# Optimization experiments

Measured on AMD Instinct MI355X. Metric: run time of the kernel, lower is better.

## Reference

```python
import jax, jax.numpy as jnp
import numpy as np

B, N, D = 32, 181, 512          # batch, num_projs (seq len), embed_dim
H, HD = 8, 64                   # heads, head_dim
DEPTH, FFN = 6, 2048            # layers, mlp_ratio*embed_dim
MAXLEN = 181                    # RPE max_len (EncoderLayer default)
LN_EPS = 1e-5


def setup_inputs() -> dict:
    key = jax.random.key(0)
    ks = jax.random.split(key, 16)
    rn = lambda k, s, sc=0.02: (jax.random.normal(k, s, jnp.float32) * sc)
    return {
        "x_0": jax.random.normal(ks[0], (B, N, D), jnp.float32),
        "max_shift": 50,
        "pos_embed": rn(ks[1], (1, N, D)),
        "qkv_w": rn(ks[2], (DEPTH, D, 3 * D)), "qkv_b": jnp.zeros((DEPTH, 3 * D), jnp.float32),
        "out_w": rn(ks[3], (DEPTH, D, D)), "out_b": jnp.zeros((DEPTH, D), jnp.float32),
        "rel_pos": jax.random.normal(ks[4], (DEPTH, 2 * MAXLEN - 1, HD), jnp.float32),
        "rpe_w": rn(ks[5], (DEPTH, HD, 1)),
        "ln1_g": jnp.ones((DEPTH, D), jnp.float32), "ln1_b": jnp.zeros((DEPTH, D), jnp.float32),
        "ffn_w1": rn(ks[6], (DEPTH, D, FFN)), "ffn_b1": jnp.zeros((DEPTH, FFN), jnp.float32),
        "ffn_w2": rn(ks[7], (DEPTH, FFN, D)), "ffn_b2": jnp.zeros((DEPTH, D), jnp.float32),
        "ln2_g": jnp.ones((DEPTH, D), jnp.float32), "ln2_b": jnp.zeros((DEPTH, D), jnp.float32),
        "mlp_w1": rn(ks[8], (D, 64)), "mlp_b1": jnp.zeros((64,), jnp.float32),
        "mlp_w2": rn(ks[9], (64, 1)), "mlp_b2": jnp.zeros((1,), jnp.float32),
    }


def _layer_norm(x, g, b):
    m = jnp.mean(x, -1, keepdims=True)
    v = jnp.mean((x - m) ** 2, -1, keepdims=True)
    return (x - m) * jax.lax.rsqrt(v + LN_EPS) * g + b


def reference(x_0, max_shift, pos_embed, qkv_w, qkv_b, out_w, out_b, rel_pos, rpe_w,
              ln1_g, ln1_b, ffn_w1, ffn_b1, ffn_w2, ffn_b2, ln2_g, ln2_b,
              mlp_w1, mlp_b1, mlp_w2, mlp_b2):
    Bb, T, L = x_0.shape
    n_head = H
    hd = L // n_head
    scale = hd ** -0.5
    max_len = (rel_pos.shape[1] + 1) // 2
    # relative position index table [T, T]
    idx = jnp.arange(T)[None, :] - jnp.arange(T)[:, None] + (max_len - 1)

    x = x_0 + pos_embed
    depth = qkv_w.shape[0]
    for i in range(depth):
        # --- MHA with relative position bias ---
        qkv = (x @ qkv_w[i] + qkv_b[i]).reshape(Bb, T, 3, n_head, hd)
        q, k, v = qkv[:, :, 0], qkv[:, :, 1], qkv[:, :, 2]   # [B,T,H,hd]
        scores = jnp.einsum('bqhd,bkhd->bhqk', q, k) * scale
        bias = (rel_pos[i][idx] @ rpe_w[i])[..., 0]          # [T,T]
        scores = scores + bias[None, None]
        w = jax.nn.softmax(scores, axis=-1)
        attn = jnp.einsum('bhqk,bkhd->bqhd', w, v).reshape(Bb, T, L)
        attn = attn @ out_w[i] + out_b[i]
        x = _layer_norm(x + attn, ln1_g[i], ln1_b[i])
        # --- FFN ---
        h = jax.nn.gelu(x @ ffn_w1[i] + ffn_b1[i], approximate=False)
        h = h @ ffn_w2[i] + ffn_b2[i]
        x = _layer_norm(x + h, ln2_g[i], ln2_b[i])

    # per-projection shift head
    shift = jax.nn.relu(x @ mlp_w1 + mlp_b1) @ mlp_w2 + mlp_b2   # [B,T,1]

    # --- SpatialTransformer: bilinear warp along L only (flow[:,0] == 0) ---
    grid_y = 2.0 * (jnp.arange(T, dtype=jnp.float32) / (T - 1) - 0.5)   # [T]
    grid_x = 2.0 * (jnp.arange(L, dtype=jnp.float32) / (L - 1) - 0.5)   # [L]
    flow_x = shift * max_shift / (L // 2)                               # [B,T,1]
    gx = grid_x[None, None, :] + flow_x                                 # [B,T,L]
    # unnormalize (align_corners=False), border padding -> clamp coords
    ix = jnp.clip(((gx + 1.0) * L - 1.0) / 2.0, 0.0, L - 1.0)
    iy = jnp.clip(((grid_y + 1.0) * T - 1.0) / 2.0, 0.0, T - 1.0)       # [T]
    ix0f = jnp.floor(ix); wx = ix - ix0f
    iy0f = jnp.floor(iy); wy = iy - iy0f
    ix0 = jnp.clip(ix0f.astype(jnp.int32), 0, L - 1)
    ix1 = jnp.clip(ix0 + 1, 0, L - 1)
    iy0 = jnp.clip(iy0f.astype(jnp.int32), 0, T - 1)
    iy1 = jnp.clip(iy0 + 1, 0, T - 1)
    bidx = jnp.arange(Bb)[:, None, None]
    iy0b, iy1b = iy0[None, :, None], iy1[None, :, None]
    v00 = x_0[bidx, iy0b, ix0]; v01 = x_0[bidx, iy0b, ix1]
    v10 = x_0[bidx, iy1b, ix0]; v11 = x_0[bidx, iy1b, ix1]
    wyb = wy[None, :, None]
    warped = (1 - wyb) * ((1 - wx) * v00 + wx * v01) + wyb * ((1 - wx) * v10 + wx * v11)
    return shift, warped
```

## Files before the change

kernel.cpp:

```cpp
#include <hip/hip_runtime.h>
#include <hip/hip_bf16.h>
#include <math.h>

#define M_ROWS 5792
#define NTOK 181
#define NLAYER 6

typedef __attribute__((ext_vector_type(8))) _Float16 f16x8;
typedef __attribute__((ext_vector_type(4))) float f32x4;
typedef __attribute__((ext_vector_type(16))) float f32x16;

__device__ __forceinline__ ushort f2h(float f) {
    union { _Float16 h; ushort u; } v;
    v.h = (_Float16)f;
    return v.u;
}
__device__ __forceinline__ float h2f(ushort u) {
    union { ushort u; _Float16 h; } v; v.u = u;
    return (float)v.h;
}
__device__ __forceinline__ float gelu_f(float v) {
    return 0.5f * v * (1.0f + erff(v * 0.70710678118654752f));
}
__device__ __forceinline__ void async16(const void* g, void* l) {
    __builtin_amdgcn_global_load_lds((const __attribute__((address_space(1))) void*)g,
                                     (__attribute__((address_space(3))) void*)l, 16, 0, 0);
}

__global__ __launch_bounds__(256) void wt_kernel(const float* __restrict__ W,
                                                 ushort* __restrict__ Wt, int K, int N) {
    __shared__ float t[64][65];
    const size_t ls = (size_t)blockIdx.z * K * N;
    const float* Wl = W + ls;
    ushort* Wtl = Wt + ls;
    const int k0 = blockIdx.x * 64, n0 = blockIdx.y * 64;
    const int tr = threadIdx.x >> 6, tc = threadIdx.x & 63;
    #pragma unroll
    for (int i = 0; i < 16; ++i) {
        const int r = i * 4 + tr;
        t[r][tc] = Wl[(size_t)(k0 + r) * N + n0 + tc];
    }
    __syncthreads();
    #pragma unroll
    for (int i = 0; i < 16; ++i) {
        const int r = i * 4 + tr;
        Wtl[(size_t)(n0 + r) * K + k0 + tc] = f2h(t[tc][r]);
    }
}

__global__ void add_pos_kernel(const float* __restrict__ x0, const float* __restrict__ pos,
                               float* __restrict__ x, ushort* __restrict__ xb) {
    int idx = blockIdx.x * 256 + threadIdx.x;
    const int total = M_ROWS * 128;
    if (idx >= total) return;
    int col = idx & 127;
    int m   = idx >> 7;
    int t   = m % NTOK;
    float4 a = ((const float4*)x0)[idx];
    float4 p = ((const float4*)pos)[t * 128 + col];
    a.x += p.x; a.y += p.y; a.z += p.z; a.w += p.w;
    ((float4*)x)[idx] = a;
    ((ushort4*)xb)[idx] = make_ushort4(f2h(a.x), f2h(a.y), f2h(a.z), f2h(a.w));
}

template<int BM, int EPI, int SK>
__global__ __launch_bounds__(256) void mfma_gemm(const ushort* __restrict__ A,
                                                 const ushort* __restrict__ Bt,
                                                 const float* __restrict__ bias,
                                                 void* __restrict__ Cv,
                                                 int M, int K, int N) {
    constexpr int MREP = BM / 32;
    __shared__ __align__(16) ushort sA[2][BM * 32];
    __shared__ __align__(16) ushort sB[2][128 * 32];

    const int NC  = N >> 7;
    const int NR  = (M + BM - 1) / BM;
    const int NRP = (NR + 7) & ~7;
    const int PSB = NRP * NC;
    const int gid = blockIdx.x;
    const int sk  = (SK > 1) ? gid / PSB : 0;
    const int j   = (SK > 1) ? gid % PSB : gid;
    const int r   = (j / (8 * NC)) * 8 + (j & 7);
    const int c   = (j % (8 * NC)) >> 3;
    if (r >= NR) return;

    const int tid = threadIdx.x;
    const int lane = tid & 63;
    const int w = tid >> 6;
    const int wr = w >> 1, wc = w & 1;
    const int row0 = r * BM, col0 = c * 128;
    const int wbase = tid & ~63;

    f32x4 acc[MREP][4];
    const f32x4 zero = {0.f, 0.f, 0.f, 0.f};
    #pragma unroll
    for (int m = 0; m < MREP; ++m)
        #pragma unroll
        for (int n = 0; n < 4; ++n) acc[m][n] = zero;

    auto stage = [&](int buf, int kt) {
        const int k0 = kt << 5;
        #pragma unroll
        for (int i = 0; i < BM / 64; ++i) {
            const int s = i * 256 + tid;
            const int row = s >> 2;
            const int kbl = (s & 3) ^ ((row >> 1) & 3);
            int gr = row0 + row; if (gr > M - 1) gr = M - 1;
            async16(A + (size_t)gr * K + k0 + (kbl << 3),
                    &sA[buf][(i * 256 + wbase) * 8]);
        }
        #pragma unroll
        for (int i = 0; i < 2; ++i) {
            const int s = i * 256 + tid;
            const int nr = s >> 2;
            const int kbl = (s & 3) ^ ((nr >> 1) & 3);
            async16(Bt + (size_t)(col0 + nr) * K + k0 + (kbl << 3),
                    &sB[buf][(i * 256 + wbase) * 8]);
        }
    };

    const int NIT = (K / SK) >> 5;
    const int kt0 = sk * NIT;
    stage(0, kt0);
    const int l15 = lane & 15, kb = lane >> 4;
    for (int it = 0; it < NIT; ++it) {
        __syncthreads();
        if (it + 1 < NIT) stage((it + 1) & 1, kt0 + it + 1);
        const int buf = it & 1;
        f16x8 af[MREP], bfr[4];
        #pragma unroll
        for (int m = 0; m < MREP; ++m) {
            const int rr = wr * (BM / 2) + m * 16 + l15;
            af[m] = *(const f16x8*)&sA[buf][rr * 32 + ((kb ^ ((rr >> 1) & 3)) << 3)];
        }
        #pragma unroll
        for (int n = 0; n < 4; ++n) {
            const int rr = wc * 64 + n * 16 + l15;
            bfr[n] = *(const f16x8*)&sB[buf][rr * 32 + ((kb ^ ((rr >> 1) & 3)) << 3)];
        }
        #pragma unroll
        for (int m = 0; m < MREP; ++m)
            #pragma unroll
            for (int n = 0; n < 4; ++n)
                acc[m][n] = __builtin_amdgcn_mfma_f32_16x16x32_f16(af[m], bfr[n], acc[m][n], 0, 0, 0);
    }

    const int crow = row0 + wr * (BM / 2) + (lane >> 4) * 4;
    const int ccol = col0 + wc * 64 + l15;
    ushort* outh = (ushort*)Cv + (size_t)sk * M * N;
    #pragma unroll
    for (int m = 0; m < MREP; ++m)
        #pragma unroll
        for (int n = 0; n < 4; ++n) {
            const int gc = ccol + n * 16;
            const float bv = (SK == 1 || sk == 0) ? bias[gc] : 0.f;
            #pragma unroll
            for (int rr = 0; rr < 4; ++rr) {
                const int gr = crow + m * 16 + rr;
                if (gr < M) {
                    float v = acc[m][n][rr] + bv;
                    if (EPI == 1)      outh[(size_t)gr * N + gc] = f2h(gelu_f(v));
                    else if (EPI == 2) outh[(size_t)gr * N + gc] = f2h(v);
                    else               ((float*)Cv)[(size_t)gr * N + gc] = v;
                }
            }
        }
}

__global__ __launch_bounds__(256) void head_mfma(const ushort* __restrict__ A,
                                                 const ushort* __restrict__ Bt,
                                                 const float* __restrict__ b1,
                                                 const float* __restrict__ w2,
                                                 const float* __restrict__ b2,
                                                 float* __restrict__ shift) {
    const int M = M_ROWS, K = 512;
    __shared__ __align__(16) ushort sA[2][128 * 32];
    __shared__ __align__(16) ushort sB[2][64 * 32];
    const int tid = threadIdx.x;
    const int lane = tid & 63;
    const int w = tid >> 6;
    const int row0 = blockIdx.x * 128;
    const int wbase = tid & ~63;

    f32x4 acc[2][4];
    const f32x4 zero = {0.f, 0.f, 0.f, 0.f};
    #pragma unroll
    for (int m = 0; m < 2; ++m)
        #pragma unroll
        for (int n = 0; n < 4; ++n) acc[m][n] = zero;

    auto stage = [&](int buf, int kt) {
        const int k0 = kt << 5;
        #pragma unroll
        for (int i = 0; i < 2; ++i) {
            const int s = i * 256 + tid;
            const int row = s >> 2;
            const int kbl = (s & 3) ^ ((row >> 1) & 3);
            int gr = row0 + row; if (gr > M - 1) gr = M - 1;
            async16(A + (size_t)gr * K + k0 + (kbl << 3),
                    &sA[buf][(i * 256 + wbase) * 8]);
        }
        {
            const int s = tid;
            const int nr = s >> 2;
            const int kbl = (s & 3) ^ ((nr >> 1) & 3);
            async16(Bt + (size_t)nr * K + k0 + (kbl << 3),
                    &sB[buf][wbase * 8]);
        }
    };

    stage(0, 0);
    const int l15 = lane & 15, kb = lane >> 4;
    for (int it = 0; it < 16; ++it) {
        __syncthreads();
        if (it + 1 < 16) stage((it + 1) & 1, it + 1);
        const int buf = it & 1;
        f16x8 af[2], bfr[4];
        #pragma unroll
        for (int m = 0; m < 2; ++m) {
            const int r = w * 32 + m * 16 + l15;
            af[m] = *(const f16x8*)&sA[buf][r * 32 + ((kb ^ ((r >> 1) & 3)) << 3)];
        }
        #pragma unroll
        for (int n = 0; n < 4; ++n) {
            const int r = n * 16 + l15;
            bfr[n] = *(const f16x8*)&sB[buf][r * 32 + ((kb ^ ((r >> 1) & 3)) << 3)];
        }
        #pragma unroll
        for (int m = 0; m < 2; ++m)
            #pragma unroll
            for (int n = 0; n < 4; ++n)
                acc[m][n] = __builtin_amdgcn_mfma_f32_16x16x32_f16(af[m], bfr[n], acc[m][n], 0, 0, 0);
    }

    const float b2v = b2[0];
    float b1v[4], w2v[4];
    #pragma unroll
    for (int n = 0; n < 4; ++n) {
        const int c = n * 16 + l15;
        b1v[n] = b1[c];
        w2v[n] = w2[c];
    }
    #pragma unroll
    for (int m = 0; m < 2; ++m) {
        #pragma unroll
        for (int r = 0; r < 4; ++r) {
            float p = 0.f;
            #pragma unroll
            for (int n = 0; n < 4; ++n)
                p += fmaxf(acc[m][n][r] + b1v[n], 0.f) * w2v[n];
            #pragma unroll
            for (int off = 1; off < 16; off <<= 1) p += __shfl_xor(p, off);
            const int gr = row0 + w * 32 + m * 16 + kb * 4 + r;
            if (l15 == 0 && gr < M) shift[gr] = p + b2v;
        }
    }
}

__global__ void rbias_kernel(const float* __restrict__ rel_pos, const float* __restrict__ rpe_w,
                             float* __restrict__ r) {
    const int l = blockIdx.y;
    int j = blockIdx.x * 64 + threadIdx.x;
    if (j >= 2 * NTOK - 1) return;
    const float* rp = rel_pos + ((size_t)l * (2 * NTOK - 1) + j) * 64;
    const float* wv = rpe_w + l * 64;
    float s = 0.f;
    #pragma unroll
    for (int d = 0; d < 64; d += 4) {
        float4 a = *(const float4*)(rp + d);
        float4 b = *(const float4*)(wv + d);
        s += a.x*b.x + a.y*b.y + a.z*b.z + a.w*b.w;
    }
    r[l * 512 + j] = s;
}

__global__ __launch_bounds__(192, 1) void attn_fused(const ushort* __restrict__ xb,
                                                     const ushort* __restrict__ Wt,
                                                     const float* __restrict__ bias,
                                                     const float* __restrict__ rb,
                                                     ushort* __restrict__ outb) {
    extern __shared__ __align__(16) char smem[];
    ushort* Ks = (ushort*)smem;
    ushort* Qs = Ks + 12288;
    ushort* vt = Qs + 12288;
    ushort* sA = vt + 12288;
    ushort* sB = sA + 12288;
    float*  rs = (float*)(smem + 122880);

    const int b = blockIdx.x >> 3;
    const int h = blockIdx.x & 7;
    const int tid = threadIdx.x, lane = tid & 63, w = tid >> 6;
    const int l31 = lane & 31, hi = lane >> 5;
    const int l15 = lane & 15, kb = lane >> 4;
    const int wbase = tid & ~63;

    for (int i = tid; i < 416; i += 192) {
        int j = i - 32;
        rs[i] = (j >= 0 && j < 2 * NTOK - 1) ? rb[j] : 0.f;
    }

    const ushort* Arow = xb + (size_t)(b * NTOK) * 512;

    auto stage = [&](int buf, int it) {
        const int k0 = it << 5;
        #pragma unroll
        for (int i = 0; i < 4; ++i) {
            const int s = i * 192 + tid;
            const int row = s >> 2;
            const int kbl = (s & 3) ^ ((row >> 1) & 3);
            const int gr = row < NTOK ? row : NTOK - 1;
            async16(Arow + (size_t)gr * 512 + k0 + (kbl << 3),
                    &sA[buf * 6144 + (i * 192 + wbase) * 8]);
        }
        #pragma unroll
        for (int i = 0; i < 4; ++i) {
            const int s = i * 192 + tid;
            const int n = s >> 2;
            const int kbl = (s & 3) ^ ((n >> 1) & 3);
            const int wrow = (n >> 6) * 512 + h * 64 + (n & 63);
            async16(Wt + (size_t)wrow * 512 + k0 + (kbl << 3),
                    &sB[buf * 6144 + (i * 192 + wbase) * 8]);
        }
    };

    f32x4 acc[48];
    const f32x4 zero = {0.f, 0.f, 0.f, 0.f};
    #pragma unroll
    for (int t = 0; t < 48; ++t) acc[t] = zero;

    stage(0, 0);
    for (int it = 0; it < 16; ++it) {
        __syncthreads();
        if (it + 1 < 16) stage((it + 1) & 1, it + 1);
        const ushort* a  = &sA[(it & 1) * 6144];
        const ushort* bw = &sB[(it & 1) * 6144];
        if (w < 2) {
            f16x8 af[12], bf[4];
            #pragma unroll
            for (int mt = 0; mt < 12; ++mt) {
                const int r = mt * 16 + l15;
                af[mt] = *(const f16x8*)&a[r * 32 + ((kb ^ ((r >> 1) & 3)) << 3)];
            }
            #pragma unroll
            for (int nt = 0; nt < 4; ++nt) {
                const int n = w * 64 + nt * 16 + l15;
                bf[nt] = *(const f16x8*)&bw[n * 32 + ((kb ^ ((n >> 1) & 3)) << 3)];
            }
            #pragma unroll
            for (int mt = 0; mt < 12; ++mt)
                #pragma unroll
                for (int nt = 0; nt < 4; ++nt)
                    acc[mt * 4 + nt] = __builtin_amdgcn_mfma_f32_16x16x32_f16(af[mt], bf[nt], acc[mt * 4 + nt], 0, 0, 0);
        } else {
            f16x8 af[4], bf[12];
            #pragma unroll
            for (int mt = 0; mt < 4; ++mt) {
                const int n = 128 + mt * 16 + l15;
                af[mt] = *(const f16x8*)&bw[n * 32 + ((kb ^ ((n >> 1) & 3)) << 3)];
            }
            #pragma unroll
            for (int nt = 0; nt < 12; ++nt) {
                const int r = nt * 16 + l15;
                bf[nt] = *(const f16x8*)&a[r * 32 + ((kb ^ ((r >> 1) & 3)) << 3)];
            }
            #pragma unroll
            for (int mt = 0; mt < 4; ++mt)
                #pragma unroll
                for (int nt = 0; nt < 12; ++nt)
                    acc[mt * 12 + nt] = __builtin_amdgcn_mfma_f32_16x16x32_f16(af[mt], bf[nt], acc[mt * 12 + nt], 0, 0, 0);
        }
    }

    if (w < 2) {
        ushort* dst = (w == 0) ? Qs : Ks;
        const int boff = w * 512 + h * 64;
        #pragma unroll
        for (int nt = 0; nt < 4; ++nt) {
            const int d = nt * 16 + l15;
            const float bv = bias[boff + d];
            #pragma unroll
            for (int mt = 0; mt < 12; ++mt)
                #pragma unroll
                for (int r = 0; r < 4; ++r) {
                    const int tok = mt * 16 + kb * 4 + r;
                    dst[tok * 64 + (((d >> 3) ^ (tok & 7)) << 3) + (d & 7)] =
                        f2h(acc[mt * 4 + nt][r] + bv);
                }
        }
    } else {
        #pragma unroll
        for (int mt = 0; mt < 4; ++mt)
            #pragma unroll
            for (int r = 0; r < 4; ++r) {
                const int d = mt * 16 + kb * 4 + r;
                const float bv = bias[1024 + h * 64 + d];
                const int sd = (d ^ (d >> 3)) & 7;
                #pragma unroll
                for (int nt = 0; nt < 12; ++nt) {
                    const int tok = nt * 16 + l15;
                    vt[d * 192 + (((tok >> 3) ^ sd) << 3) + (tok & 7)] =
                        f2h(acc[mt * 12 + nt][r] + bv);
                }
            }
    }
    __syncthreads();

    for (int qt = 0; qt < 2; ++qt) {
        const int q0 = (w + 3 * qt) * 32;
        const int q = q0 + l31;
        f16x8 qf[4];
        #pragma unroll
        for (int ds = 0; ds < 4; ++ds)
            qf[ds] = *(const f16x8*)&Qs[q * 64 + (((2 * ds + hi) ^ (q & 7)) << 3)];

        f32x16 S[6];
        #pragma unroll
        for (int kt = 0; kt < 6; ++kt)
            #pragma unroll
            for (int r = 0; r < 16; ++r) S[kt][r] = 0.f;
        __builtin_amdgcn_s_setprio(1);
        #pragma unroll
        for (int kt = 0; kt < 6; ++kt) {
            const int krow = kt * 32 + l31;
            #pragma unroll
            for (int ds = 0; ds < 4; ++ds) {
                f16x8 kf = *(const f16x8*)&Ks[krow * 64 + (((2 * ds + hi) ^ (krow & 7)) << 3)];
                S[kt] = __builtin_amdgcn_mfma_f32_32x32x16_f16(kf, qf[ds], S[kt], 0, 0, 0);
            }
        }
        __builtin_amdgcn_s_setprio(0);

        float mx = -1e30f;
        #pragma unroll
        for (int kt = 0; kt < 6; ++kt)
            #pragma unroll
            for (int r = 0; r < 16; ++r) {
                const int k = kt * 32 + (r & 3) + 8 * (r >> 2) + 4 * hi;
                float s = (k < NTOK) ? S[kt][r] * 0.125f + rs[k - q + 212] : -1e30f;
                S[kt][r] = s;
                mx = fmaxf(mx, s);
            }
        mx = fmaxf(mx, __shfl_xor(mx, 32));
        float sum = 0.f;
        #pragma unroll
        for (int kt = 0; kt < 6; ++kt)
            #pragma unroll
            for (int r = 0; r < 16; ++r) {
                float e = __expf(S[kt][r] - mx);
                S[kt][r] = e;
                sum += e;
            }
        sum += __shfl_xor(sum, 32);
        const float inv = 1.0f / sum;
        #pragma unroll
        for (int kt = 0; kt < 6; ++kt)
            #pragma unroll
            for (int r = 0; r < 16; ++r) S[kt][r] *= inv;

        f32x16 O[2];
        #pragma unroll
        for (int nt = 0; nt < 2; ++nt)
            #pragma unroll
            for (int r = 0; r < 16; ++r) O[nt][r] = 0.f;
        #pragma unroll
        for (int kt2 = 0; kt2 < 12; ++kt2) {
            const int kt = kt2 >> 1, half = kt2 & 1;
            uint p[4];
            #pragma unroll
            for (int m = 0; m < 4; ++m)
                p[m] = (uint)f2h(S[kt][8 * half + 2 * m]) |
                       ((uint)f2h(S[kt][8 * half + 2 * m + 1]) << 16);
            const uint s0l = (uint)__shfl_xor((int)p[0], 32);
            const uint s0h = (uint)__shfl_xor((int)p[1], 32);
            const uint s1l = (uint)__shfl_xor((int)p[2], 32);
            const uint s1h = (uint)__shfl_xor((int)p[3], 32);
            uint fa[4];
            if (hi == 0) { fa[0] = p[0]; fa[1] = p[1]; fa[2] = s0l; fa[3] = s0h; }
            else         { fa[0] = s1l; fa[1] = s1h; fa[2] = p[2]; fa[3] = p[3]; }
            const f16x8 pa = *(const f16x8*)fa;
            __builtin_amdgcn_s_setprio(1);
            #pragma unroll
            for (int nt = 0; nt < 2; ++nt) {
                const int d = nt * 32 + l31;
                f16x8 vf = *(const f16x8*)&vt[d * 192 + (((2 * kt2 + hi) ^ ((d ^ (d >> 3)) & 7)) << 3)];
                O[nt] = __builtin_amdgcn_mfma_f32_32x32x16_f16(pa, vf, O[nt], 0, 0, 0);
            }
            __builtin_amdgcn_s_setprio(0);
        }

        #pragma unroll
        for (int nt = 0; nt < 2; ++nt)
            #pragma unroll
            for (int r = 0; r < 16; ++r) {
                const int qr = q0 + (r & 3) + 8 * (r >> 2) + 4 * hi;
                if (qr < NTOK)
                    outb[(size_t)(b * NTOK + qr) * 512 + h * 64 + nt * 32 + l31] = f2h(O[nt][r]);
            }
    }
}

template<int NY>
__global__ __launch_bounds__(256) void lnres_kernel(float* __restrict__ x, ushort* __restrict__ xb,
                                                    const ushort* __restrict__ y,
                                                    const ushort* __restrict__ y1,
                                                    const float* __restrict__ g, const float* __restrict__ bb) {
    const int row = blockIdx.x * 4 + (threadIdx.x >> 6);
    const int l = threadIdx.x & 63;
    float* xr = x + (size_t)row * 512;
    ushort* xbr = xb + (size_t)row * 512;
    const ushort* yr = y + (size_t)row * 512;
    float4 v0 = *(const float4*)(xr + (l << 2));
    float4 v1 = *(const float4*)(xr + 256 + (l << 2));
    const ushort4 u0 = *(const ushort4*)(yr + (l << 2));
    const ushort4 u1 = *(const ushort4*)(yr + 256 + (l << 2));
    v0.x += h2f(u0.x); v0.y += h2f(u0.y); v0.z += h2f(u0.z); v0.w += h2f(u0.w);
    v1.x += h2f(u1.x); v1.y += h2f(u1.y); v1.z += h2f(u1.z); v1.w += h2f(u1.w);
    if (NY == 2) {
        const ushort* y1r = y1 + (size_t)row * 512;
        const ushort4 w0 = *(const ushort4*)(y1r + (l << 2));
        const ushort4 w1 = *(const ushort4*)(y1r + 256 + (l << 2));
        v0.x += h2f(w0.x); v0.y += h2f(w0.y); v0.z += h2f(w0.z); v0.w += h2f(w0.w);
        v1.x += h2f(w1.x); v1.y += h2f(w1.y); v1.z += h2f(w1.z); v1.w += h2f(w1.w);
    }
    float s = v0.x + v0.y + v0.z + v0.w + v1.x + v1.y + v1.z + v1.w;
    #pragma unroll
    for (int off = 32; off; off >>= 1) s += __shfl_xor(s, off);
    const float m = s * (1.0f / 512.0f);
    float d0 = v0.x - m, d1 = v0.y - m, d2 = v0.z - m, d3 = v0.w - m;
    float d4 = v1.x - m, d5 = v1.y - m, d6 = v1.z - m, d7 = v1.w - m;
    float q = d0*d0 + d1*d1 + d2*d2 + d3*d3 + d4*d4 + d5*d5 + d6*d6 + d7*d7;
    #pragma unroll
    for (int off = 32; off; off >>= 1) q += __shfl_xor(q, off);
    const float r = rsqrtf(q * (1.0f / 512.0f) + 1e-5f);
    const float4 g0 = *(const float4*)(g + (l << 2));
    const float4 g1 = *(const float4*)(g + 256 + (l << 2));
    const float4 b0 = *(const float4*)(bb + (l << 2));
    const float4 b1 = *(const float4*)(bb + 256 + (l << 2));
    float4 o0, o1;
    o0.x = d0 * r * g0.x + b0.x; o0.y = d1 * r * g0.y + b0.y;
    o0.z = d2 * r * g0.z + b0.z; o0.w = d3 * r * g0.w + b0.w;
    o1.x = d4 * r * g1.x + b1.x; o1.y = d5 * r * g1.y + b1.y;
    o1.z = d6 * r * g1.z + b1.z; o1.w = d7 * r * g1.w + b1.w;
    *(float4*)(xr + (l << 2)) = o0;
    *(float4*)(xr + 256 + (l << 2)) = o1;
    *(ushort4*)(xbr + (l << 2)) = make_ushort4(f2h(o0.x), f2h(o0.y), f2h(o0.z), f2h(o0.w));
    *(ushort4*)(xbr + 256 + (l << 2)) = make_ushort4(f2h(o1.x), f2h(o1.y), f2h(o1.z), f2h(o1.w));
}

__global__ void warp_kernel(const float* __restrict__ x0, const float* __restrict__ shift,
                            const int* __restrict__ pms, float* __restrict__ warped) {
    int idx = blockIdx.x * 256 + threadIdx.x;
    if (idx >= M_ROWS * 512) return;
    int c = idx & 511;
    int m = idx >> 9;
    int t = m % NTOK;
    int b = m / NTOK;
    float max_shift = (float)pms[0];
    float sh = shift[m];
    float flow = sh * max_shift / 256.0f;
    float gx = 2.0f * ((float)c / 511.0f - 0.5f) + flow;
    float ix = ((gx + 1.0f) * 512.0f - 1.0f) * 0.5f;
    ix = fminf(fmaxf(ix, 0.0f), 511.0f);
    float gy = 2.0f * ((float)t / 180.0f - 0.5f);
    float iy = ((gy + 1.0f) * 181.0f - 1.0f) * 0.5f;
    iy = fminf(fmaxf(iy, 0.0f), 180.0f);
    float ix0f = floorf(ix), iy0f = floorf(iy);
    float wx = ix - ix0f, wy = iy - iy0f;
    int ix0 = min(max((int)ix0f, 0), 511);
    int ix1 = min(ix0 + 1, 511);
    int iy0 = min(max((int)iy0f, 0), 180);
    int iy1 = min(iy0 + 1, 180);
    const float* xb = x0 + (size_t)b * NTOK * 512;
    float v00 = xb[iy0 * 512 + ix0], v01 = xb[iy0 * 512 + ix1];
    float v10 = xb[iy1 * 512 + ix0], v11 = xb[iy1 * 512 + ix1];
    warped[idx] = (1.f - wy) * ((1.f - wx) * v00 + wx * v01) + wy * ((1.f - wx) * v10 + wx * v11);
}

extern "C" void kernel_launch(void* const* d_in, const int* in_sizes, int n_in,
                              void* d_out, int out_size, void* d_ws, size_t ws_size,
                              hipStream_t stream) {
    const float* x0   = (const float*)d_in[0];
    const int*   pms  = (const int*)d_in[1];
    const float* pos  = (const float*)d_in[2];
    const float* qkvw = (const float*)d_in[3];
    const float* qkvb = (const float*)d_in[4];
    const float* outw = (const float*)d_in[5];
    const float* outbp= (const float*)d_in[6];
    const float* relp = (const float*)d_in[7];
    const float* rpew = (const float*)d_in[8];
    const float* ln1g = (const float*)d_in[9];
    const float* ln1b = (const float*)d_in[10];
    const float* fw1  = (const float*)d_in[11];
    const float* fb1  = (const float*)d_in[12];
    const float* fw2  = (const float*)d_in[13];
    const float* fb2  = (const float*)d_in[14];
    const float* ln2g = (const float*)d_in[15];
    const float* ln2b = (const float*)d_in[16];
    const float* mw1  = (const float*)d_in[17];
    const float* mb1  = (const float*)d_in[18];
    const float* mw2  = (const float*)d_in[19];
    const float* mb2  = (const float*)d_in[20];

    float* out = (float*)d_out;

    char* ws = (char*)d_ws;
    float*  x     = (float*)ws;
    ushort* xb    = (ushort*)(ws + 11862016);
    char*   qr    = ws + 11862016 + 5931008;
    ushort* ybuf  = (ushort*)qr;
    ushort* ybuf2 = (ushort*)(qr + 5931008);
    ushort* hbuf  = (ushort*)(qr + 11862016);
    ushort* attnb = (ushort*)(qr + 35586048);
    float*  rbias = (float*)(qr + 35586048 + 5931008);
    ushort* wts   = (ushort*)(qr + 35586048 + 5931008 + 12288);
    ushort* qkv_wt = wts;
    ushort* out_wt = qkv_wt + 6 * 1536 * 512;
    ushort* f1_wt  = out_wt + 6 * 512 * 512;
    ushort* f2_wt  = f1_wt  + 6 * 512 * 2048;
    ushort* w1t    = f2_wt  + 6 * 2048 * 512;

    static_assert(true, "");
    hipFuncSetAttribute((const void*)attn_fused,
                        hipFuncAttributeMaxDynamicSharedMemorySize, 124544);

    wt_kernel<<<dim3(8, 24, 6), 256, 0, stream>>>(qkvw, qkv_wt, 512, 1536);
    wt_kernel<<<dim3(8,  8, 6), 256, 0, stream>>>(outw, out_wt, 512, 512);
    wt_kernel<<<dim3(8, 32, 6), 256, 0, stream>>>(fw1,  f1_wt,  512, 2048);
    wt_kernel<<<dim3(32, 8, 6), 256, 0, stream>>>(fw2,  f2_wt,  2048, 512);
    wt_kernel<<<dim3(8,  1, 1), 256, 0, stream>>>(mw1,  w1t,    512, 64);
    rbias_kernel<<<dim3(6, 6), 64, 0, stream>>>(relp, rpew, rbias);

    add_pos_kernel<<<(M_ROWS * 128 + 255) / 256, 256, 0, stream>>>(x0, pos, x, xb);

    const int g_ffn1 = 96 * 16;
    const int g_np4  = 96 * 4;
    for (int i = 0; i < NLAYER; ++i) {
        attn_fused<<<256, 192, 124544, stream>>>(xb, qkv_wt + (size_t)i * 1536 * 512,
                                                 qkvb + i * 1536, rbias + i * 512, attnb);
        mfma_gemm<64, 2, 2><<<g_np4 * 2, 256, 0, stream>>>(attnb, out_wt + (size_t)i * 512 * 512,
                                                           outbp + i * 512, ybuf, M_ROWS, 512, 512);
        lnres_kernel<2><<<1448, 256, 0, stream>>>(x, xb, ybuf, ybuf2, ln1g + i * 512, ln1b + i * 512);
        mfma_gemm<64, 1, 1><<<g_ffn1, 256, 0, stream>>>(xb, f1_wt + (size_t)i * 2048 * 512,
                                                        fb1 + i * 2048, hbuf, M_ROWS, 512, 2048);
        mfma_gemm<64, 2, 2><<<g_np4 * 2, 256, 0, stream>>>(hbuf, f2_wt + (size_t)i * 512 * 2048,
                                                           fb2 + i * 512, ybuf, M_ROWS, 2048, 512);
        lnres_kernel<2><<<1448, 256, 0, stream>>>(x, xb, ybuf, ybuf2, ln2g + i * 512, ln2b + i * 512);
    }

    head_mfma<<<46, 256, 0, stream>>>(xb, w1t, mb1, mw2, mb2, out);
    warp_kernel<<<(M_ROWS * 512 + 255) / 256, 256, 0, stream>>>(x0, out, pms, out + M_ROWS);
}
```

Measured before the change: 737.3 us.

## Fuse out-proj and FFN2 GEMMs with residual add and LayerNorm

Replaces the split-K output-projection and FFN2 GEMMs plus the separate residual+LayerNorm kernel with one kernel. Each block computes a full 16x512 row tile, stages the biased result in shared memory, then applies residual add and LayerNorm in place. This removes the fp16 partial-sum round trip through global memory and two kernel launches per layer. In exchange each block streams the entire 512-column weight panel for only 16 rows, giving little weight reuse and only 362 blocks with a tall B tile per k-step, so GEMM efficiency may fall, especially for the K=2048 FFN2.

```diff
diff --git a/kernel.cpp b/kernel.cpp
--- a/kernel.cpp
+++ b/kernel.cpp
@@ -165,6 +165,114 @@
                 }
             }
         }
+}
+
+__global__ __launch_bounds__(256) void gemm_lnfull(const ushort* __restrict__ A,
+                                                   const ushort* __restrict__ Bt,
+                                                   const float* __restrict__ bias,
+                                                   float* __restrict__ x, ushort* __restrict__ xb,
+                                                   const float* __restrict__ g,
+                                                   const float* __restrict__ bb,
+                                                   int K) {
+    __shared__ __align__(16) ushort sA[2][16 * 32];
+    __shared__ __align__(16) ushort sB[2][512 * 32];
+    float* sLN = (float*)&sB[0][0];
+
+    const int tid = threadIdx.x;
+    const int lane = tid & 63;
+    const int w = tid >> 6;
+    const int l15 = lane & 15, kb = lane >> 4;
+    const int wbase = tid & ~63;
+    const int row0 = blockIdx.x * 16;
+
+    f32x4 acc[8];
+    const f32x4 zero = {0.f, 0.f, 0.f, 0.f};
+    #pragma unroll
+    for (int n = 0; n < 8; ++n) acc[n] = zero;
+
+    auto stage = [&](int buf, int kt) {
+        const int k0 = kt << 5;
+        if (w == 0) {
+            const int row = lane >> 2;
+            const int kbl = (lane & 3) ^ ((row >> 1) & 3);
+            async16(A + (size_t)(row0 + row) * K + k0 + (kbl << 3), &sA[buf]);
+        }
+        #pragma unroll
+        for (int i = 0; i < 8; ++i) {
+            const int s = i * 256 + tid;
+            const int nr = s >> 2;
+            const int kbl = (s & 3) ^ ((nr >> 1) & 3);
+            async16(Bt + (size_t)nr * K + k0 + (kbl << 3),
+                    &sB[buf][(i * 256 + wbase) * 8]);
+        }
+    };
+
+    const int NIT = K >> 5;
+    stage(0, 0);
+    for (int it = 0; it < NIT; ++it) {
+        __syncthreads();
+        if (it + 1 < NIT) stage((it + 1) & 1, it + 1);
+        const int buf = it & 1;
+        f16x8 af = *(const f16x8*)&sA[buf][l15 * 32 + ((kb ^ ((l15 >> 1) & 3)) << 3)];
+        f16x8 bf[8];
+        #pragma unroll
+        for (int n = 0; n < 8; ++n) {
+            const int nr = w * 128 + n * 16 + l15;
+            bf[n] = *(const f16x8*)&sB[buf][nr * 32 + ((kb ^ ((nr >> 1) & 3)) << 3)];
+        }
+        #pragma unroll
+        for (int n = 0; n < 8; ++n)
+            acc[n] = __builtin_amdgcn_mfma_f32_16x16x32_f16(af, bf[n], acc[n], 0, 0, 0);
+    }
+    __syncthreads();
+
+    #pragma unroll
+    for (int n = 0; n < 8; ++n) {
+        const int col = w * 128 + n * 16 + l15;
+        const float bv = bias[col];
+        #pragma unroll
+        for (int r = 0; r < 4; ++r)
+            sLN[(kb * 4 + r) * 520 + col] = acc[n][r] + bv;
+    }
+    __syncthreads();
+
+    #pragma unroll 1
+    for (int r4 = 0; r4 < 4; ++r4) {
+        const int row = w * 4 + r4;
+        const int gr = row0 + row;
+        float* xr = x + (size_t)gr * 512;
+        ushort* xbr = xb + (size_t)gr * 512;
+        const float* yr = &sLN[row * 520];
+        float4 v0 = *(const float4*)(xr + (lane << 2));
+        float4 v1 = *(const float4*)(xr + 256 + (lane << 2));
+        const float4 u0 = *(const float4*)(yr + (lane << 2));
+        const float4 u1 = *(const float4*)(yr + 256 + (lane << 2));
+        v0.x += u0.x; v0.y += u0.y; v0.z += u0.z; v0.w += u0.w;
+        v1.x += u1.x; v1.y += u1.y; v1.z += u1.z; v1.w += u1.w;
+        float s = v0.x + v0.y + v0.z + v0.w + v1.x + v1.y + v1.z + v1.w;
+        #pragma unroll
+        for (int off = 32; off; off >>= 1) s += __shfl_xor(s, off);
+        const float m = s * (1.0f / 512.0f);
+        float d0 = v0.x - m, d1 = v0.y - m, d2 = v0.z - m, d3 = v0.w - m;
+        float d4 = v1.x - m, d5 = v1.y - m, d6 = v1.z - m, d7 = v1.w - m;
+        float q = d0*d0 + d1*d1 + d2*d2 + d3*d3 + d4*d4 + d5*d5 + d6*d6 + d7*d7;
+        #pragma unroll
+        for (int off = 32; off; off >>= 1) q += __shfl_xor(q, off);
+        const float rq = rsqrtf(q * (1.0f / 512.0f) + 1e-5f);
+        const float4 g0 = *(const float4*)(g + (lane << 2));
+        const float4 g1 = *(const float4*)(g + 256 + (lane << 2));
+        const float4 b0 = *(const float4*)(bb + (lane << 2));
+        const float4 b1 = *(const float4*)(bb + 256 + (lane << 2));
+        float4 o0, o1;
+        o0.x = d0 * rq * g0.x + b0.x; o0.y = d1 * rq * g0.y + b0.y;
+        o0.z = d2 * rq * g0.z + b0.z; o0.w = d3 * rq * g0.w + b0.w;
+        o1.x = d4 * rq * g1.x + b1.x; o1.y = d5 * rq * g1.y + b1.y;
+        o1.z = d6 * rq * g1.z + b1.z; o1.w = d7 * rq * g1.w + b1.w;
+        *(float4*)(xr + (lane << 2)) = o0;
+        *(float4*)(xr + 256 + (lane << 2)) = o1;
+        *(ushort4*)(xbr + (lane << 2)) = make_ushort4(f2h(o0.x), f2h(o0.y), f2h(o0.z), f2h(o0.w));
+        *(ushort4*)(xbr + 256 + (lane << 2)) = make_ushort4(f2h(o1.x), f2h(o1.y), f2h(o1.z), f2h(o1.w));
+    }
 }
 
 __global__ __launch_bounds__(256) void head_mfma(const ushort* __restrict__ A,
@@ -497,54 +605,6 @@
                     outb[(size_t)(b * NTOK + qr) * 512 + h * 64 + nt * 32 + l31] = f2h(O[nt][r]);
             }
     }
-}
-
-template<int NY>
-__global__ __launch_bounds__(256) void lnres_kernel(float* __restrict__ x, ushort* __restrict__ xb,
-                                                    const ushort* __restrict__ y,
-                                                    const ushort* __restrict__ y1,
-                                                    const float* __restrict__ g, const float* __restrict__ bb) {
-    const int row = blockIdx.x * 4 + (threadIdx.x >> 6);
-    const int l = threadIdx.x & 63;
-    float* xr = x + (size_t)row * 512;
-    ushort* xbr = xb + (size_t)row * 512;
-    const ushort* yr = y + (size_t)row * 512;
-    float4 v0 = *(const float4*)(xr + (l << 2));
-    float4 v1 = *(const float4*)(xr + 256 + (l << 2));
-    const ushort4 u0 = *(const ushort4*)(yr + (l << 2));
-    const ushort4 u1 = *(const ushort4*)(yr + 256 + (l << 2));
-    v0.x += h2f(u0.x); v0.y += h2f(u0.y); v0.z += h2f(u0.z); v0.w += h2f(u0.w);
-    v1.x += h2f(u1.x); v1.y += h2f(u1.y); v1.z += h2f(u1.z); v1.w += h2f(u1.w);
-    if (NY == 2) {
-        const ushort* y1r = y1 + (size_t)row * 512;
-        const ushort4 w0 = *(const ushort4*)(y1r + (l << 2));
-        const ushort4 w1 = *(const ushort4*)(y1r + 256 + (l << 2));
-        v0.x += h2f(w0.x); v0.y += h2f(w0.y); v0.z += h2f(w0.z); v0.w += h2f(w0.w);
-        v1.x += h2f(w1.x); v1.y += h2f(w1.y); v1.z += h2f(w1.z); v1.w += h2f(w1.w);
-    }
-    float s = v0.x + v0.y + v0.z + v0.w + v1.x + v1.y + v1.z + v1.w;
-    #pragma unroll
-    for (int off = 32; off; off >>= 1) s += __shfl_xor(s, off);
-    const float m = s * (1.0f / 512.0f);
-    float d0 = v0.x - m, d1 = v0.y - m, d2 = v0.z - m, d3 = v0.w - m;
-    float d4 = v1.x - m, d5 = v1.y - m, d6 = v1.z - m, d7 = v1.w - m;
-    float q = d0*d0 + d1*d1 + d2*d2 + d3*d3 + d4*d4 + d5*d5 + d6*d6 + d7*d7;
-    #pragma unroll
-    for (int off = 32; off; off >>= 1) q += __shfl_xor(q, off);
-    const float r = rsqrtf(q * (1.0f / 512.0f) + 1e-5f);
-    const float4 g0 = *(const float4*)(g + (l << 2));
-    const float4 g1 = *(const float4*)(g + 256 + (l << 2));
-    const float4 b0 = *(const float4*)(bb + (l << 2));
-    const float4 b1 = *(const float4*)(bb + 256 + (l << 2));
-    float4 o0, o1;
-    o0.x = d0 * r * g0.x + b0.x; o0.y = d1 * r * g0.y + b0.y;
-    o0.z = d2 * r * g0.z + b0.z; o0.w = d3 * r * g0.w + b0.w;
-    o1.x = d4 * r * g1.x + b1.x; o1.y = d5 * r * g1.y + b1.y;
-    o1.z = d6 * r * g1.z + b1.z; o1.w = d7 * r * g1.w + b1.w;
-    *(float4*)(xr + (l << 2)) = o0;
-    *(float4*)(xr + 256 + (l << 2)) = o1;
-    *(ushort4*)(xbr + (l << 2)) = make_ushort4(f2h(o0.x), f2h(o0.y), f2h(o0.z), f2h(o0.w));
-    *(ushort4*)(xbr + 256 + (l << 2)) = make_ushort4(f2h(o1.x), f2h(o1.y), f2h(o1.z), f2h(o1.w));
 }
 
 __global__ void warp_kernel(const float* __restrict__ x0, const float* __restrict__ shift,
@@ -607,8 +667,6 @@
     float*  x     = (float*)ws;
     ushort* xb    = (ushort*)(ws + 11862016);
     char*   qr    = ws + 11862016 + 5931008;
-    ushort* ybuf  = (ushort*)qr;
-    ushort* ybuf2 = (ushort*)(qr + 5931008);
     ushort* hbuf  = (ushort*)(qr + 11862016);
     ushort* attnb = (ushort*)(qr + 35586048);
     float*  rbias = (float*)(qr + 35586048 + 5931008);
@@ -619,7 +677,6 @@
     ushort* f2_wt  = f1_wt  + 6 * 512 * 2048;
     ushort* w1t    = f2_wt  + 6 * 2048 * 512;
 
-    static_assert(true, "");
     hipFuncSetAttribute((const void*)attn_fused,
                         hipFuncAttributeMaxDynamicSharedMemorySize, 124544);
 
@@ -633,18 +690,17 @@
     add_pos_kernel<<<(M_ROWS * 128 + 255) / 256, 256, 0, stream>>>(x0, pos, x, xb);
 
     const int g_ffn1 = 96 * 16;
-    const int g_np4  = 96 * 4;
     for (int i = 0; i < NLAYER; ++i) {
         attn_fused<<<256, 192, 124544, stream>>>(xb, qkv_wt + (size_t)i * 1536 * 512,
                                                  qkvb + i * 1536, rbias + i * 512, attnb);
-        mfma_gemm<64, 2, 2><<<g_np4 * 2, 256, 0, stream>>>(attnb, out_wt + (size_t)i * 512 * 512,
-                                                           outbp + i * 512, ybuf, M_ROWS, 512, 512);
-        lnres_kernel<2><<<1448, 256, 0, stream>>>(x, xb, ybuf, ybuf2, ln1g + i * 512, ln1b + i * 512);
+        gemm_lnfull<<<362, 256, 0, stream>>>(attnb, out_wt + (size_t)i * 512 * 512,
+                                             outbp + i * 512, x, xb,
+                                             ln1g + i * 512, ln1b + i * 512, 512);
         mfma_gemm<64, 1, 1><<<g_ffn1, 256, 0, stream>>>(xb, f1_wt + (size_t)i * 2048 * 512,
                                                         fb1 + i * 2048, hbuf, M_ROWS, 512, 2048);
-        mfma_gemm<64, 2, 2><<<g_np4 * 2, 256, 0, stream>>>(hbuf, f2_wt + (size_t)i * 512 * 2048,
-                                                           fb2 + i * 512, ybuf, M_ROWS, 2048, 512);
-        lnres_kernel<2><<<1448, 256, 0, stream>>>(x, xb, ybuf, ybuf2, ln2g + i * 512, ln2b + i * 512);
+        gemm_lnfull<<<362, 256, 0, stream>>>(hbuf, f2_wt + (size_t)i * 512 * 2048,
+                                             fb2 + i * 512, x, xb,
+                                             ln2g + i * 512, ln2b + i * 512, 2048);
     }
 
     head_mfma<<<46, 256, 0, stream>>>(xb, w1t, mb1, mw2, mb2, out);
```

Measured after the change: 967.9 us. 31.3% more time.
